# Performance work log

Measured on AMD Instinct MI355X. Metric: run time of the kernel, lower is better.

## Reference

```python
import jax, jax.numpy as jnp
import numpy as np

B, T, D_IN, D_OUT, N_HEAD = 2, 2048, 1024, 1024, 16
HEAD_DIM = D_OUT // N_HEAD


def setup_inputs() -> dict:
    key = jax.random.key(0)
    k1, k2, k3, k4 = jax.random.split(key, 4)
    s = 0.02  # init scale for weights
    return {
        "x": jax.random.normal(k1, (B, T, D_IN), jnp.float32),
        "Wq": jax.random.normal(k2, (D_OUT, D_IN), jnp.float32) * s,
        "Wk": jax.random.normal(k3, (D_OUT, D_IN), jnp.float32) * s,
        "Wv": jax.random.normal(k4, (D_OUT, D_IN), jnp.float32) * s,
    }


def reference(x, Wq, Wk, Wv):
    b, t, _ = x.shape
    h, hd = N_HEAD, HEAD_DIM
    # Linear projections (torch Linear: x @ W.T), split heads -> [b,h,t,hd]
    q = (x @ Wq.T).reshape(b, t, h, hd).transpose(0, 2, 1, 3)
    k = (x @ Wk.T).reshape(b, t, h, hd).transpose(0, 2, 1, 3)
    v = (x @ Wv.T).reshape(b, t, h, hd).transpose(0, 2, 1, 3)
    # raw scores [b,h,t,t], causal mask BEFORE scaling (as in source)
    omega = jnp.einsum("bhqd,bhkd->bhqk", q, k)
    causal = jnp.triu(jnp.ones((t, t), dtype=bool), k=1)
    omega = jnp.where(causal, -jnp.inf, omega)
    attw = jax.nn.softmax(omega / jnp.sqrt(jnp.asarray(hd, omega.dtype)), axis=-1)
    ctx = jnp.einsum("bhqk,bhkd->bhqd", attw, v)  # [b,h,t,hd]
    # Faithful to source: transpose(2,3) then view(B,T,d_out)
    out = jnp.swapaxes(ctx, 2, 3).reshape(b, t, D_OUT)
    return out
```

## Files before the change

### kernel.cpp

```cpp
#include <hip/hip_runtime.h>
#include <hip/hip_bf16.h>
#include <stdint.h>

typedef __attribute__((ext_vector_type(8))) short s16x8;
typedef __attribute__((ext_vector_type(4))) float f32x4;

#define T_   2048
#define NH   16
#define HD   64
#define DIN  1024
#define SCALE_LOG2 0.18033688011112042f

#define MFMA32(a, b, c) __builtin_amdgcn_mfma_f32_16x16x32_bf16(a, b, c, 0, 0, 0)

__device__ __forceinline__ unsigned short f2bf(float f) {
  union { float f; uint32_t u; } c; c.f = f;
  uint32_t u = c.u;
  return (unsigned short)((u + 0x7FFFu + ((u >> 16) & 1u)) >> 16);
}

__device__ __forceinline__ uint32_t pk_bf16(float a, float b) {
  __hip_bfloat162 h = __float22bfloat162_rn(make_float2(a, b));
  return *reinterpret_cast<uint32_t*>(&h);
}

#define GLL(gp, lp) __builtin_amdgcn_global_load_lds( \
    (__attribute__((address_space(1))) void*)(gp),    \
    (__attribute__((address_space(3))) void*)(lp), 16, 0, 0)

__global__ __launch_bounds__(256) void cvt_kernel(
    const float* __restrict__ x,  const float* __restrict__ wq,
    const float* __restrict__ wk, const float* __restrict__ wv,
    unsigned short* __restrict__ xb, unsigned short* __restrict__ wb) {
  int i = (blockIdx.x * 256 + threadIdx.x) * 4;
  float4 v;
  unsigned short* dp;
  if (i < 4194304) {
    v = *(const float4*)(x + i);
    dp = xb + i;
  } else {
    int j = i - 4194304;
    int seg = j >> 20, r = j & 1048575;
    const float* w = (seg == 0) ? wq : (seg == 1) ? wk : wv;
    v = *(const float4*)(w + r);
    dp = wb + j;
  }
  ushort4 o;
  o.x = f2bf(v.x); o.y = f2bf(v.y); o.z = f2bf(v.z); o.w = f2bf(v.w);
  *(ushort4*)dp = o;
}

__global__ __launch_bounds__(256) void qkv_gemm(
    const unsigned short* __restrict__ A, const unsigned short* __restrict__ Bm,
    unsigned short* __restrict__ qkv) {
  __shared__ __attribute__((aligned(16))) unsigned short Alds[64 * 64];
  __shared__ __attribute__((aligned(16))) unsigned short Blds[128 * 64];
  const int tid = threadIdx.x;
  const int lane = tid & 63, wave = tid >> 6;
  const int wm = wave >> 1, wn = wave & 1;
  const int m0 = blockIdx.y * 64, n0 = blockIdx.x * 128;

  f32x4 acc[2][4] = {};

  const int srA = wave * 16 + (lane >> 3);
  const int srB = wave * 32 + (lane >> 3);
  const int scol = (((lane & 7) ^ ((lane >> 3) & 7))) * 8;
  const unsigned short* ag = A  + (size_t)(m0 + srA) * DIN + scol;
  const unsigned short* bg = Bm + (size_t)(n0 + srB) * DIN + scol;
  unsigned short* al = &Alds[wave * 16 * 64];
  unsigned short* bl = &Blds[wave * 32 * 64];

  const int l16 = lane & 15, quad = lane >> 4;
  const int sw = l16 & 7;

  for (int k0 = 0; k0 < DIN; k0 += 64) {
    __syncthreads();
#pragma unroll
    for (int i = 0; i < 2; i++)
      GLL(ag + (size_t)i * 8 * DIN + k0, al + i * 512);
#pragma unroll
    for (int i = 0; i < 4; i++)
      GLL(bg + (size_t)i * 8 * DIN + k0, bl + i * 512);
    __syncthreads();
#pragma unroll
    for (int ks = 0; ks < 2; ks++) {
      const int cl = ((ks * 4 + quad) ^ sw) * 8;
      s16x8 af[2], bf[4];
#pragma unroll
      for (int mt = 0; mt < 2; mt++)
        af[mt] = *(const s16x8*)&Alds[(wm * 32 + mt * 16 + l16) * 64 + cl];
#pragma unroll
      for (int nt = 0; nt < 4; nt++)
        bf[nt] = *(const s16x8*)&Blds[(wn * 64 + nt * 16 + l16) * 64 + cl];
#pragma unroll
      for (int mt = 0; mt < 2; mt++)
#pragma unroll
        for (int nt = 0; nt < 4; nt++)
          acc[mt][nt] = MFMA32(af[mt], bf[nt], acc[mt][nt]);
    }
  }

#pragma unroll
  for (int mt = 0; mt < 2; mt++) {
    int mbase = m0 + wm * 32 + mt * 16 + (quad << 2);
    int b = mbase >> 11, t = mbase & 2047;
#pragma unroll
    for (int nt = 0; nt < 4; nt++) {
      int n = n0 + wn * 64 + nt * 16 + l16;
      int sel = n >> 10, h = (n >> 6) & 15, d = n & 63;
      int bh = b * NH + h;
      if (sel == 2) {
        ushort4 pk;
        pk.x = f2bf(acc[mt][nt][0]); pk.y = f2bf(acc[mt][nt][1]);
        pk.z = f2bf(acc[mt][nt][2]); pk.w = f2bf(acc[mt][nt][3]);
        *(ushort4*)&qkv[8388608 + (size_t)(bh * HD + d) * T_ + t] = pk;
      } else {
        float qs = (sel == 0) ? SCALE_LOG2 : 1.f;
#pragma unroll
        for (int r = 0; r < 4; r++)
          qkv[(size_t)sel * 4194304 + (size_t)(bh * T_ + t + r) * HD + d] =
              f2bf(acc[mt][nt][r] * qs);
      }
    }
  }
}

__device__ __forceinline__ void tile_step(
    const unsigned short* Klds, const unsigned short* Vt,
    unsigned short* Plds, const s16x8 qf0, const s16x8 qf1,
    f32x4 o[4], f32x4& lacc,
    const int l16, const int quad, const int swl, const int wave,
    const bool diag) {
  f32x4 s[4] = {};
#pragma unroll
  for (int kk = 0; kk < 2; kk++) {
    const int cl = ((kk * 4 + quad) ^ swl) * 8;
    const s16x8 q = kk ? qf1 : qf0;
#pragma unroll
    for (int mt = 0; mt < 4; mt++) {
      s16x8 kf = *(const s16x8*)&Klds[(mt * 16 + l16) * 64 + cl];
      s[mt] = MFMA32(kf, q, s[mt]);
    }
  }

  uint32_t* prow = (uint32_t*)&Plds[(wave * 16 + l16) * 64];
  if (!diag) {
#pragma unroll
    for (int mt = 0; mt < 4; mt++) {
      float p0 = exp2f(s[mt][0]);
      float p1 = exp2f(s[mt][1]);
      float p2 = exp2f(s[mt][2]);
      float p3 = exp2f(s[mt][3]);
      *(uint2*)&prow[(((2 * mt + (quad >> 1)) ^ swl) << 2) + (quad & 1) * 2] =
          make_uint2(pk_bf16(p0, p1), pk_bf16(p2, p3));
    }
  } else {
    const int lim = wave * 16 + l16;
#pragma unroll
    for (int mt = 0; mt < 4; mt++) {
      const int kb = mt * 16 + quad * 4;
      float p0 = (kb + 0 <= lim) ? exp2f(s[mt][0]) : 0.f;
      float p1 = (kb + 1 <= lim) ? exp2f(s[mt][1]) : 0.f;
      float p2 = (kb + 2 <= lim) ? exp2f(s[mt][2]) : 0.f;
      float p3 = (kb + 3 <= lim) ? exp2f(s[mt][3]) : 0.f;
      *(uint2*)&prow[(((2 * mt + (quad >> 1)) ^ swl) << 2) + (quad & 1) * 2] =
          make_uint2(pk_bf16(p0, p1), pk_bf16(p2, p3));
    }
  }

  const s16x8 onesf = {0x3F80, 0x3F80, 0x3F80, 0x3F80,
                       0x3F80, 0x3F80, 0x3F80, 0x3F80};
  const unsigned short* prd = &Plds[(wave * 16 + l16) * 64];
#pragma unroll
  for (int kk = 0; kk < 2; kk++) {
    const int cl = ((kk * 4 + quad) ^ swl) * 8;
    s16x8 pf = *(const s16x8*)&prd[cl];
    lacc = MFMA32(pf, onesf, lacc);
#pragma unroll
    for (int dt = 0; dt < 4; dt++) {
      s16x8 vf = *(const s16x8*)&Vt[(dt * 16 + l16) * 64 + cl];
      o[dt] = MFMA32(pf, vf, o[dt]);
    }
  }
}

__global__ __launch_bounds__(256) void attn_kernel(
    const unsigned short* __restrict__ qkv, float* __restrict__ out,
    float* __restrict__ op, float* __restrict__ lp) {
  __shared__ __attribute__((aligned(16))) unsigned short Klds[64 * 64];
  __shared__ __attribute__((aligned(16))) unsigned short Vt[64 * 64];
  __shared__ __attribute__((aligned(16))) unsigned short Plds[64 * 64];

  const int tid = threadIdx.x;
  const int lane = tid & 63, wave = tid >> 6;
  const int l16 = lane & 15, quad = lane >> 4;
  const int swl = l16 & 7;
  const int bh = blockIdx.x;

  const int y = blockIdx.y;
  int j;
  if (y < 18) {
    j = (y == 0) ? 15 : ((y == 17) ? 47 : 15 + y);
  } else {
    const int z = y - 18, L = 15 - (z >> 1);
    j = (z & 1) ? (L - 1) : (L + 31);
  }
  int qt, kt0, kt1, hi;
  bool split;
  if (j < 16)      { qt = j;      kt0 = 0;  kt1 = j;  split = false; hi = 0; }
  else if (j < 32) { qt = j;      kt0 = 0;  kt1 = 15; split = true;  hi = 0; }
  else             { qt = j - 16; kt0 = 16; kt1 = qt; split = true;  hi = 1; }

  const size_t bh_off = (size_t)bh * (T_ * HD);
  const unsigned short* Q  = qkv + bh_off;
  const unsigned short* Kb = qkv + 4194304 + bh_off;
  const unsigned short* Vb = qkv + 8388608 + bh_off;

  s16x8 qf0, qf1;
  {
    const unsigned short* qp =
        Q + (size_t)(qt * 64 + wave * 16 + l16) * HD + quad * 8;
    qf0 = *(const s16x8*)(qp);
    qf1 = *(const s16x8*)(qp + 32);
  }

  const int sr = tid >> 3;
  const int sc = (tid & 7) * 8;
  const int swc = (((tid & 7) ^ (sr & 7))) * 8;

  s16x8 kr0 = *(const s16x8*)&Kb[(size_t)(kt0 * 64 + sr) * HD + sc];
  s16x8 kr1 = *(const s16x8*)&Kb[(size_t)(kt0 * 64 + sr + 32) * HD + sc];
  s16x8 vr0 = *(const s16x8*)&Vb[(size_t)sr * T_ + kt0 * 64 + sc];
  s16x8 vr1 = *(const s16x8*)&Vb[(size_t)(sr + 32) * T_ + kt0 * 64 + sc];

  f32x4 o[4] = {};
  f32x4 lacc = {};

  for (int kt = kt0; kt <= kt1; kt++) {
    __syncthreads();
    *(s16x8*)&Klds[sr * 64 + swc] = kr0;
    *(s16x8*)&Klds[(sr + 32) * 64 + swc] = kr1;
    *(s16x8*)&Vt[sr * 64 + swc] = vr0;
    *(s16x8*)&Vt[(sr + 32) * 64 + swc] = vr1;
    if (kt < kt1) {
      const unsigned short* kp = Kb + (size_t)(kt + 1) * 64 * HD;
      const unsigned short* vp = Vb + (kt + 1) * 64;
      kr0 = *(const s16x8*)&kp[(size_t)sr * HD + sc];
      kr1 = *(const s16x8*)&kp[(size_t)(sr + 32) * HD + sc];
      vr0 = *(const s16x8*)&vp[(size_t)sr * T_ + sc];
      vr1 = *(const s16x8*)&vp[(size_t)(sr + 32) * T_ + sc];
    }
    __syncthreads();

    tile_step(Klds, Vt, Plds, qf0, qf1, o, lacc, l16, quad, swl, wave,
              kt == qt);
  }

  if (!split) {
    f32x4 inv;
#pragma unroll
    for (int r = 0; r < 4; r++) inv[r] = 1.f / lacc[r];
#pragma unroll
    for (int dt = 0; dt < 4; dt++) {
      float4 v = make_float4(o[dt][0] * inv[0], o[dt][1] * inv[1],
                             o[dt][2] * inv[2], o[dt][3] * inv[3]);
      *(float4*)(out + (size_t)bh * (HD * T_) + (size_t)(dt * 16 + l16) * T_ +
                 qt * 64 + wave * 16 + quad * 4) = v;
    }
  } else {
    const int slot = ((bh * 16 + (qt - 16)) << 1) + hi;
    float* Op = op + (size_t)slot * 4096;
    float* Lp = lp + (size_t)slot * 64;
#pragma unroll
    for (int dt = 0; dt < 4; dt++) {
      float4 v = make_float4(o[dt][0], o[dt][1], o[dt][2], o[dt][3]);
      *(float4*)(Op + (dt * 16 + l16) * 64 + wave * 16 + quad * 4) = v;
    }
    if (l16 == 0) {
#pragma unroll
      for (int r = 0; r < 4; r++) Lp[wave * 16 + quad * 4 + r] = lacc[r];
    }
  }
}

__global__ __launch_bounds__(256) void combine_kernel(
    const float* __restrict__ op, const float* __restrict__ lp,
    float* __restrict__ out) {
  const int bh = blockIdx.x, j2 = blockIdx.y;
  const int slot = (bh * 16 + j2) << 1;
  const float* Olo = op + (size_t)slot * 4096;
  const float* Ohi = Olo + 4096;
  const float* Llo = lp + (size_t)slot * 64;
  const int t = threadIdx.x;
  const int q = t & 63, d0 = (t >> 6) * 16;
  const float inv = 1.f / (Llo[q] + Llo[64 + q]);
  float* ob = out + (size_t)bh * (HD * T_) + (size_t)(j2 + 16) * 64 + q;
#pragma unroll
  for (int dd = 0; dd < 16; dd++) {
    const int d = d0 + dd;
    ob[(size_t)d * T_] = (Olo[d * 64 + q] + Ohi[d * 64 + q]) * inv;
  }
}

extern "C" void kernel_launch(void* const* d_in, const int* in_sizes, int n_in,
                              void* d_out, int out_size, void* d_ws, size_t ws_size,
                              hipStream_t stream) {
  const float* x  = (const float*)d_in[0];
  const float* wq = (const float*)d_in[1];
  const float* wk = (const float*)d_in[2];
  const float* wv = (const float*)d_in[3];
  float* out = (float*)d_out;

  unsigned short* xb  = (unsigned short*)d_ws;
  unsigned short* wb  = xb + 4194304;
  unsigned short* qkv = wb + 3145728;
  float* op = (float*)(qkv + 12582912);
  float* lp = op + 4194304;

  cvt_kernel<<<7168, 256, 0, stream>>>(x, wq, wk, wv, xb, wb);
  dim3 g1(24, 64);
  qkv_gemm<<<g1, 256, 0, stream>>>(xb, wb, qkv);
  dim3 g2(32, 48);
  attn_kernel<<<g2, 256, 0, stream>>>(qkv, out, op, lp);
  dim3 g3(32, 16);
  combine_kernel<<<g3, 256, 0, stream>>>(op, lp, out);
}
```

Before: 150.4 us.

## Split causal attention KV range into 8-tile chunks for finer load balancing

Replaces the two-way split of long query rows with a split into chunks of at most 8 key tiles, so every attention block does at most 8 tiles of work, and raises the grid from 48 to 80 blocks per head. The combine kernel now sums a variable number (2-4) of partial outputs and denominators per query tile. This is meant to shorten the critical-path block and balance the wave of work across CUs, at the cost of more partial-result traffic to workspace and a heavier combine pass.

```diff
diff --git a/kernel.cpp b/kernel.cpp
--- a/kernel.cpp
+++ b/kernel.cpp
@@ -125,6 +125,11 @@
   }
 }
 
+__device__ __forceinline__ int soff(int qt) {
+  return (qt < 16) ? (qt - 8) * 2
+                   : (qt < 24) ? 16 + (qt - 16) * 3 : 40 + (qt - 24) * 4;
+}
+
 __device__ __forceinline__ void tile_step(
     const unsigned short* Klds, const unsigned short* Vt,
     unsigned short* Plds, const s16x8 qf0, const s16x8 qf1,
@@ -198,18 +203,15 @@
   const int bh = blockIdx.x;
 
   const int y = blockIdx.y;
-  int j;
-  if (y < 18) {
-    j = (y == 0) ? 15 : ((y == 17) ? 47 : 15 + y);
-  } else {
-    const int z = y - 18, L = 15 - (z >> 1);
-    j = (z & 1) ? (L - 1) : (L + 31);
-  }
-  int qt, kt0, kt1, hi;
-  bool split;
-  if (j < 16)      { qt = j;      kt0 = 0;  kt1 = j;  split = false; hi = 0; }
-  else if (j < 32) { qt = j;      kt0 = 0;  kt1 = 15; split = true;  hi = 0; }
-  else             { qt = j - 16; kt0 = 16; kt1 = qt; split = true;  hi = 1; }
+  int qt, c;
+  if (y < 25)       { c = 0; qt = 7 + y; }
+  else if (y < 42)  { c = 1; qt = 15 + (y - 25); }
+  else if (y < 51)  { c = 2; qt = 23 + (y - 42); }
+  else if (y == 51) { c = 3; qt = 31; }
+  else { const int i = y - 52; c = i & 3; qt = 8 * c + (6 - (i >> 2)); }
+  const int kt0 = 8 * c;
+  const int kt1 = min(kt0 + 7, qt);
+  const bool split = (qt >= 8);
 
   const size_t bh_off = (size_t)bh * (T_ * HD);
   const unsigned short* Q  = qkv + bh_off;
@@ -268,7 +270,7 @@
                  qt * 64 + wave * 16 + quad * 4) = v;
     }
   } else {
-    const int slot = ((bh * 16 + (qt - 16)) << 1) + hi;
+    const int slot = bh * 72 + soff(qt) + c;
     float* Op = op + (size_t)slot * 4096;
     float* Lp = lp + (size_t)slot * 64;
 #pragma unroll
@@ -286,19 +288,22 @@
 __global__ __launch_bounds__(256) void combine_kernel(
     const float* __restrict__ op, const float* __restrict__ lp,
     float* __restrict__ out) {
-  const int bh = blockIdx.x, j2 = blockIdx.y;
-  const int slot = (bh * 16 + j2) << 1;
-  const float* Olo = op + (size_t)slot * 4096;
-  const float* Ohi = Olo + 4096;
-  const float* Llo = lp + (size_t)slot * 64;
+  const int bh = blockIdx.x, qt = blockIdx.y + 8;
+  const int nc = (qt + 8) >> 3;
+  const int base = bh * 72 + soff(qt);
+  const float* Op = op + (size_t)base * 4096;
+  const float* Lp = lp + (size_t)base * 64;
   const int t = threadIdx.x;
   const int q = t & 63, d0 = (t >> 6) * 16;
-  const float inv = 1.f / (Llo[q] + Llo[64 + q]);
-  float* ob = out + (size_t)bh * (HD * T_) + (size_t)(j2 + 16) * 64 + q;
-#pragma unroll
+  float lsum = 0.f;
+  for (int ci = 0; ci < nc; ci++) lsum += Lp[ci * 64 + q];
+  const float inv = 1.f / lsum;
+  float* ob = out + (size_t)bh * (HD * T_) + (size_t)qt * 64 + q;
   for (int dd = 0; dd < 16; dd++) {
     const int d = d0 + dd;
-    ob[(size_t)d * T_] = (Olo[d * 64 + q] + Ohi[d * 64 + q]) * inv;
+    float acc = 0.f;
+    for (int ci = 0; ci < nc; ci++) acc += Op[ci * 4096 + d * 64 + q];
+    ob[(size_t)d * T_] = acc * inv;
   }
 }
 
@@ -315,13 +320,13 @@
   unsigned short* wb  = xb + 4194304;
   unsigned short* qkv = wb + 3145728;
   float* op = (float*)(qkv + 12582912);
-  float* lp = op + 4194304;
+  float* lp = op + 9437184;
 
   cvt_kernel<<<7168, 256, 0, stream>>>(x, wq, wk, wv, xb, wb);
   dim3 g1(24, 64);
   qkv_gemm<<<g1, 256, 0, stream>>>(xb, wb, qkv);
-  dim3 g2(32, 48);
+  dim3 g2(32, 80);
   attn_kernel<<<g2, 256, 0, stream>>>(qkv, out, op, lp);
-  dim3 g3(32, 16);
+  dim3 g3(32, 24);
   combine_kernel<<<g3, 256, 0, stream>>>(op, lp, out);
 }
```

Result: slower. 170.2 us (+13.1%).
